# Optimization experiments

Hardware: AMD Instinct MI355X
Metric: run time of the kernel (lower is better)

The kernel has to match this reference:

```python
import jax, jax.numpy as jnp
import numpy as np

B, S, D, H, NL, DF = 32, 512, 512, 8, 6, 2048
E = D // H
EPS = 1e-5

def _pos_emb(s, d):
    pos = np.arange(s, dtype=np.float32)[:, None]
    div = np.exp(np.arange(0, d, 2, dtype=np.float32) * (-np.log(10000.0) / d))
    pe = np.zeros((s, d), np.float32)
    pe[:, 0::2] = np.sin(pos * div)
    pe[:, 1::2] = np.cos(pos * div)
    return jnp.asarray(pe)

PE = _pos_emb(S, D)

def _ln(x, g, b):
    m = jnp.mean(x, -1, keepdims=True)
    v = jnp.var(x, -1, keepdims=True)
    return (x - m) * jax.lax.rsqrt(v + EPS) * g + b

def _cconv(x, w):
    # x: [B, C, L]; w: [O, C, 3]; Conv1d kernel=3, circular padding=1, no bias
    xp = jnp.concatenate([x[..., -1:], x, x[..., :1]], axis=-1)
    return jax.lax.conv_general_dilated(xp, w, (1,), 'VALID', dimension_numbers=('NCH', 'OIH', 'NCH'))

def _projector(x, stats, wc, w1, b1, w2, b2, w3):
    # x: [B, S, C]; stats: [B, 1, C] -> [B, out_dim]
    y = _cconv(x, wc)                                                 # [B, 1, C]
    y = jnp.concatenate([y, stats], axis=1).reshape(x.shape[0], -1)   # [B, 2C]
    y = jax.nn.relu(y @ w1.T + b1)
    y = jax.nn.relu(y @ w2.T + b2)
    return y @ w3.T

def setup_inputs():
    key = jax.random.key(0)
    ks = iter(jax.random.split(key, 48))
    r = lambda *s: jax.random.normal(next(ks), s, jnp.float32) * 0.02
    z = lambda *s: jnp.zeros(s, jnp.float32)
    o = lambda *s: jnp.ones(s, jnp.float32)
    return {
        'x_enc': jax.random.normal(next(ks), (B, S, 2), jnp.float32),
        'W_emb': r(D, 2, 3),
        'Wq': r(NL, D, D), 'bq': z(NL, D),
        'Wk': r(NL, D, D), 'bk': z(NL, D),
        'Wv': r(NL, D, D), 'bv': z(NL, D),
        'Wo': r(NL, D, D), 'bo': z(NL, D),
        'Wc1': r(NL, DF, D), 'bc1': z(NL, DF),
        'Wc2': r(NL, D, DF), 'bc2': z(NL, D),
        'g1': o(NL, D), 'be1': z(NL, D),
        'g2': o(NL, D), 'be2': z(NL, D),
        'gn': o(D), 'bn': z(D),
        'Wout': r(1, D), 'bout': z(1),
        'Wtc': r(1, S, 3), 'Wt1': r(128, 4), 'bt1': z(128), 'Wt2': r(128, 128), 'bt2': z(128), 'Wt3': r(1, 128),
        'Wdc': r(1, S, 3), 'Wd1': r(128, 4), 'bd1': z(128), 'Wd2': r(128, 128), 'bd2': z(128), 'Wd3': r(S, 128),
    }

def reference(x_enc, W_emb, Wq, bq, Wk, bk, Wv, bv, Wo, bo, Wc1, bc1, Wc2, bc2,
              g1, be1, g2, be2, gn, bn, Wout, bout,
              Wtc, Wt1, bt1, Wt2, bt2, Wt3, Wdc, Wd1, bd1, Wd2, bd2, Wd3):
    b = x_enc.shape[0]
    # de-stationary statistics (detached in the original)
    x_raw = jax.lax.stop_gradient(x_enc)
    mean_enc = jax.lax.stop_gradient(jnp.mean(x_enc, 1, keepdims=True))          # [B,1,2]
    std_enc = jax.lax.stop_gradient(jnp.sqrt(jnp.var(x_enc, 1, keepdims=True) + EPS))  # [B,1,2]
    tau = jnp.exp(_projector(x_raw, std_enc, Wtc, Wt1, bt1, Wt2, bt2, Wt3))      # [B,1]
    delta = _projector(x_raw, mean_enc, Wdc, Wd1, bd1, Wd2, bd2, Wd3)            # [B,S]
    tau4 = tau[:, :, None, None]       # [B,1,1,1]
    delta4 = delta[:, None, None, :]   # [B,1,1,S]

    # DataEmbedding: token conv (circular) + sinusoidal positional embedding
    x = _cconv(x_enc.transpose(0, 2, 1), W_emb).transpose(0, 2, 1) + PE[None]    # [B,S,D]

    scale = 1.0 / jnp.sqrt(jnp.float32(E))
    for l in range(NL):
        q = (x @ Wq[l].T + bq[l]).reshape(b, S, H, E)
        k = (x @ Wk[l].T + bk[l]).reshape(b, S, H, E)
        v = (x @ Wv[l].T + bv[l]).reshape(b, S, H, E)
        # DSAttention: rescale scores by tau, shift by delta, then scaled softmax
        scores = jnp.einsum('blhe,bshe->bhls', q, k) * tau4 + delta4
        A = jax.nn.softmax(scale * scores, axis=-1)
        attn = jnp.einsum('bhls,bshe->blhe', A, v).reshape(b, S, D)
        x = _ln(x + attn @ Wo[l].T + bo[l], g1[l], be1[l])
        y = jax.nn.gelu(x @ Wc1[l].T + bc1[l], approximate=False)
        y = y @ Wc2[l].T + bc2[l]
        x = _ln(x + y, g2[l], be2[l])
    x = _ln(x, gn, bn)
    out = jax.nn.gelu(x, approximate=False) @ Wout.T + bout  # [B,S,1]
    return out[..., 0]  # squeeze(-1) -> [B,S]
```

## Files before the change

### kernel.cpp

```cpp
#include <hip/hip_runtime.h>
#include <math.h>

#define Bb 32
#define Ss 512
#define Dd 512
#define Hh 8
#define NLn 6
#define DFf 2048

typedef unsigned short u16;
typedef __attribute__((ext_vector_type(8))) short bf16x8;
typedef __attribute__((ext_vector_type(4))) float f32x4;

__device__ __forceinline__ u16 f2bf(float f){
  union { float f; unsigned u; } x; x.f = f;
  return (u16)((x.u + 0x7fffu + ((x.u >> 16) & 1u)) >> 16);
}
__device__ __forceinline__ float gelu_f(float x){
  return 0.5f * x * (1.0f + erff(x * 0.7071067811865475f));
}
__device__ __forceinline__ f32x4 mfma16(bf16x8 a, bf16x8 b, f32x4 c){
  return __builtin_amdgcn_mfma_f32_16x16x32_bf16(a, b, c, 0, 0, 0);
}
__device__ __forceinline__ void gload16(const void* g, void* l){
  void* gg = (void*)g;
  __builtin_amdgcn_global_load_lds((__attribute__((address_space(1))) void*)gg,
                                   (__attribute__((address_space(3))) void*)l, 16, 0, 0);
}

__global__ void cast_kernel(const float* __restrict__ src, u16* __restrict__ dst, int n){
  int i = (blockIdx.x * 256 + threadIdx.x) * 4;
  if (i < n){
    float4 v = *(const float4*)&src[i];
    ushort4 o; o.x = f2bf(v.x); o.y = f2bf(v.y); o.z = f2bf(v.z); o.w = f2bf(v.w);
    *(ushort4*)&dst[i] = o;
  }
}

__global__ void cast_qkv_kernel(const float* __restrict__ src, u16* __restrict__ dst, int blk){
  int i = (blockIdx.x * 256 + threadIdx.x) * 4;
  if (i < NLn*Dd*Dd){
    int l = i >> 18, r = i & (Dd*Dd - 1);
    float4 v = *(const float4*)&src[i];
    ushort4 o; o.x = f2bf(v.x); o.y = f2bf(v.y); o.z = f2bf(v.z); o.w = f2bf(v.w);
    *(ushort4*)&dst[(size_t)l*(3*Dd*Dd) + (size_t)blk*Dd*Dd + r] = o;
  }
}

__global__ void bias_concat_kernel(const float* __restrict__ bq, const float* __restrict__ bk,
                                   const float* __restrict__ bv, float* __restrict__ dst){
  int i = blockIdx.x*256 + threadIdx.x;
  if (i < NLn*Dd){
    int l = i >> 9, r = i & 511;
    float* d = dst + (size_t)l*1536;
    d[r] = bq[i]; d[512+r] = bk[i]; d[1024+r] = bv[i];
  }
}

#define SCL 0.180336880542795f
__global__ void proj_kernel(const float* __restrict__ x_enc,
                            const float* __restrict__ Wtc, const float* __restrict__ Wt1, const float* __restrict__ bt1,
                            const float* __restrict__ Wt2, const float* __restrict__ bt2, const float* __restrict__ Wt3,
                            const float* __restrict__ Wdc, const float* __restrict__ Wd1, const float* __restrict__ bd1,
                            const float* __restrict__ Wd2, const float* __restrict__ bd2, const float* __restrict__ Wd3,
                            float* __restrict__ tau2, float* __restrict__ delta2){
  const int b = blockIdx.x, t = threadIdx.x;
  __shared__ float red[8][128];
  __shared__ float fv[8];
  __shared__ float ftau[4], fdel[4], h1t[128], h1d[128], h2t[128], h2d[128];
  float s0=0,s1=0,q0=0,q1=0,tc0=0,tc1=0,dc0=0,dc1=0;
  for (int s = t; s < Ss; s += 128){
    float x0 = x_enc[(b*Ss + s)*2 + 0];
    float x1 = x_enc[(b*Ss + s)*2 + 1];
    float wt0 = Wtc[s*3], wt1v = Wtc[s*3+1], wt2v = Wtc[s*3+2];
    float wd0 = Wdc[s*3], wd1v = Wdc[s*3+1], wd2v = Wdc[s*3+2];
    s0 += x0; s1 += x1; q0 += x0*x0; q1 += x1*x1;
    tc0 += x1*(wt0+wt2v) + x0*wt1v;
    tc1 += x0*(wt0+wt2v) + x1*wt1v;
    dc0 += x1*(wd0+wd2v) + x0*wd1v;
    dc1 += x0*(wd0+wd2v) + x1*wd1v;
  }
  red[0][t]=s0; red[1][t]=s1; red[2][t]=q0; red[3][t]=q1;
  red[4][t]=tc0; red[5][t]=tc1; red[6][t]=dc0; red[7][t]=dc1;
  __syncthreads();
  if (t < 8){ float a = 0; for (int i = 0; i < 128; i++) a += red[t][i]; fv[t] = a; }
  __syncthreads();
  if (t == 0){
    float m0 = fv[0]/Ss, m1 = fv[1]/Ss;
    float v0 = fv[2]/Ss - m0*m0, v1 = fv[3]/Ss - m1*m1;
    ftau[0]=fv[4]; ftau[1]=fv[5]; ftau[2]=sqrtf(v0+1e-5f); ftau[3]=sqrtf(v1+1e-5f);
    fdel[0]=fv[6]; fdel[1]=fv[7]; fdel[2]=m0; fdel[3]=m1;
  }
  __syncthreads();
  {
    float a = bt1[t], ad = bd1[t];
    #pragma unroll
    for (int j = 0; j < 4; j++){ a += Wt1[t*4+j]*ftau[j]; ad += Wd1[t*4+j]*fdel[j]; }
    h1t[t] = fmaxf(a, 0.f); h1d[t] = fmaxf(ad, 0.f);
  }
  __syncthreads();
  {
    float a = bt2[t], ad = bd2[t];
    for (int j = 0; j < 128; j++){ a += Wt2[t*128+j]*h1t[j]; ad += Wd2[t*128+j]*h1d[j]; }
    h2t[t] = fmaxf(a, 0.f); h2d[t] = fmaxf(ad, 0.f);
  }
  __syncthreads();
  if (t == 0){
    float z = 0; for (int j = 0; j < 128; j++) z += Wt3[j]*h2t[j];
    tau2[b] = expf(z) * SCL;
  }
  for (int s = t; s < Ss; s += 128){
    float z = 0; for (int j = 0; j < 128; j++) z += Wd3[s*128+j]*h2d[j];
    delta2[b*Ss + s] = z * SCL - 16.0f;
  }
}

__global__ void embed_kernel(const float* __restrict__ xe, const float* __restrict__ Wemb,
                             float* __restrict__ xf, u16* __restrict__ xb){
  const int bs = blockIdx.x;
  const int b = bs >> 9, s = bs & 511;
  const int t = threadIdx.x;
  const int sm = (s + 511) & 511, sp = (s + 1) & 511;
  const float xm0 = xe[(b*Ss + sm)*2],   xm1 = xe[(b*Ss + sm)*2 + 1];
  const float x00 = xe[(b*Ss + s )*2],   x01 = xe[(b*Ss + s )*2 + 1];
  const float xp0 = xe[(b*Ss + sp)*2],   xp1 = xe[(b*Ss + sp)*2 + 1];
  #pragma unroll
  for (int dd = 0; dd < 4; dd++){
    const int d = t*4 + dd;
    const float* wd = Wemb + d*6;
    float a = xm0*wd[0] + x00*wd[1] + xp0*wd[2]
            + xm1*wd[3] + x01*wd[4] + xp1*wd[5];
    const int i2 = d & ~1;
    float div = expf((float)i2 * (-9.210340371976184f / 512.0f));
    float ang = (float)s * div;
    float pe = (d & 1) ? cosf(ang) : sinf(ang);
    float v = a + pe;
    xf[(size_t)bs*Dd + d] = v;
    xb[(size_t)bs*Dd + d] = f2bf(v);
  }
}

template<int EPI>
__global__ __launch_bounds__(256) void gemm_bt(const u16* __restrict__ A, const u16* __restrict__ W,
                                               const float* __restrict__ bias, void* __restrict__ Cv,
                                               int M, int N, int K){
  __shared__ __attribute__((aligned(16))) u16 As[128*32];
  __shared__ __attribute__((aligned(16))) u16 Bs[128*32];
  const int tid = threadIdx.x;
  const int w = tid >> 6, l = tid & 63;
  const int wr = w >> 1, wc = w & 1;
  const long bm0 = (long)blockIdx.y * 128;
  const long bn0 = (long)blockIdx.x * 128;
  const int lr = l >> 2, lc = l & 3;
  const u16* Ag = A + (bm0 + w*32 + lr) * (long)K + lc*8;
  const u16* Bg = W + (bn0 + w*32 + lr) * (long)K + lc*8;
  u16* AsW = As + w*1024;
  u16* BsW = Bs + w*1024;
  f32x4 acc[4][4] = {};
  const int aro = wr*64 + (l & 15);
  const int bro = wc*64 + (l & 15);
  const int k8 = (l >> 4) * 8;
  for (int kt = 0; kt < K; kt += 32){
    gload16(Ag + kt,               AsW);
    gload16(Ag + kt + 16*(long)K,  AsW + 512);
    gload16(Bg + kt,               BsW);
    gload16(Bg + kt + 16*(long)K,  BsW + 512);
    __syncthreads();
    bf16x8 af[4], bfv[4];
    #pragma unroll
    for (int mi = 0; mi < 4; mi++) af[mi] = *(const bf16x8*)&As[(aro + mi*16)*32 + k8];
    #pragma unroll
    for (int ni = 0; ni < 4; ni++) bfv[ni] = *(const bf16x8*)&Bs[(bro + ni*16)*32 + k8];
    #pragma unroll
    for (int mi = 0; mi < 4; mi++)
      #pragma unroll
      for (int ni = 0; ni < 4; ni++)
        acc[mi][ni] = mfma16(af[mi], bfv[ni], acc[mi][ni]);
    __syncthreads();
  }
  const long rbase = bm0 + wr*64 + (l >> 4)*4;
  const int cbase = (int)bn0 + wc*64 + (l & 15);
  #pragma unroll
  for (int ni = 0; ni < 4; ni++){
    const int c = cbase + ni*16;
    const float bvv = bias[c];
    #pragma unroll
    for (int mi = 0; mi < 4; mi++){
      #pragma unroll
      for (int j = 0; j < 4; j++){
        float v = acc[mi][ni][j] + bvv;
        if (EPI == 2) v = gelu_f(v);
        const size_t idx = (size_t)(rbase + mi*16 + j) * N + c;
        if (EPI == 0) ((float*)Cv)[idx] = v;
        else          ((u16*)Cv)[idx]  = f2bf(v);
      }
    }
  }
}

__global__ __launch_bounds__(512, 2) void attn_kernel(const u16* __restrict__ qkv,
                                                      const float* __restrict__ tau2,
                                                      const float* __restrict__ delta2,
                                                      u16* __restrict__ Ob){
  const int bid = blockIdx.x;
  const int h = bid & 7, b = bid >> 3;
  const int t = threadIdx.x, w = t >> 6, l = t & 63;
  const int l15 = l & 15, l4 = l >> 4;
  __shared__ __attribute__((aligned(16))) u16 Ks[512*64];
  __shared__ __attribute__((aligned(16))) u16 Vt[64*520];
  __shared__ __attribute__((aligned(16))) u16 Ps[8][16*72];
  const size_t qkvbase = ((size_t)b*Ss)*1536 + h*64;
  {
    const u16* Kg = qkv + qkvbase + 512  + (size_t)t*1536;
    const u16* Vg = qkv + qkvbase + 1024 + (size_t)t*1536;
    #pragma unroll
    for (int c = 0; c < 8; c++){
      bf16x8 kv = *(const bf16x8*)&Kg[c*8];
      const int byte = t*128 + ((c*16) ^ ((t & 7) << 4));
      *(bf16x8*)((char*)Ks + byte) = kv;
    }
    union { bf16x8 v[8]; u16 e[64]; } vv;
    #pragma unroll
    for (int c = 0; c < 8; c++) vv.v[c] = *(const bf16x8*)&Vg[c*8];
    #pragma unroll
    for (int e = 0; e < 64; e++) Vt[e*520 + t] = vv.e[e];
  }
  const int q0 = w*64;
  bf16x8 qa[4][2];
  #pragma unroll
  for (int mi = 0; mi < 4; mi++)
    #pragma unroll
    for (int ks = 0; ks < 2; ks++)
      qa[mi][ks] = *(const bf16x8*)&qkv[qkvbase + (size_t)(q0 + mi*16 + l15)*1536 + ks*32 + l4*8];
  const float ts = tau2[b];
  bf16x8 ones8;
  #pragma unroll
  for (int i = 0; i < 8; i++) ones8[i] = (short)0x3F80;
  __syncthreads();

  f32x4 Oa[4][4] = {};
  f32x4 Ls[4] = {};
  u16* PsW = Ps[w];
  for (int kt = 0; kt < 8; kt++){
    f32x4 sc[4][4] = {};
    #pragma unroll
    for (int ni = 0; ni < 4; ni++){
      const int krow = kt*64 + ni*16 + l15;
      const int swz = (krow & 7) << 4;
      bf16x8 kf0 = *(const bf16x8*)((const char*)Ks + krow*128 + ((l4*16)      ^ swz));
      bf16x8 kf1 = *(const bf16x8*)((const char*)Ks + krow*128 + ((64 + l4*16) ^ swz));
      #pragma unroll
      for (int mi = 0; mi < 4; mi++){
        sc[mi][ni] = mfma16(qa[mi][0], kf0, sc[mi][ni]);
        sc[mi][ni] = mfma16(qa[mi][1], kf1, sc[mi][ni]);
      }
    }
    float dl[4];
    #pragma unroll
    for (int ni = 0; ni < 4; ni++) dl[ni] = delta2[b*Ss + kt*64 + ni*16 + l15];
    bf16x8 pa[4][2];
    #pragma unroll
    for (int mi = 0; mi < 4; mi++){
      #pragma unroll
      for (int ni = 0; ni < 4; ni++){
        #pragma unroll
        for (int j = 0; j < 4; j++){
          float p = exp2f(ts * sc[mi][ni][j] + dl[ni]);
          PsW[(l4*4 + j)*72 + ni*16 + l15] = f2bf(p);
        }
      }
      pa[mi][0] = *(const bf16x8*)&PsW[l15*72 +      l4*8];
      pa[mi][1] = *(const bf16x8*)&PsW[l15*72 + 32 + l4*8];
    }
    #pragma unroll
    for (int ni = 0; ni < 4; ni++){
      const int vrow = ni*16 + l15;
      bf16x8 vf0 = *(const bf16x8*)&Vt[vrow*520 + kt*64 +      l4*8];
      bf16x8 vf1 = *(const bf16x8*)&Vt[vrow*520 + kt*64 + 32 + l4*8];
      #pragma unroll
      for (int mi = 0; mi < 4; mi++){
        Oa[mi][ni] = mfma16(pa[mi][0], vf0, Oa[mi][ni]);
        Oa[mi][ni] = mfma16(pa[mi][1], vf1, Oa[mi][ni]);
      }
    }
    #pragma unroll
    for (int mi = 0; mi < 4; mi++){
      Ls[mi] = mfma16(pa[mi][0], ones8, Ls[mi]);
      Ls[mi] = mfma16(pa[mi][1], ones8, Ls[mi]);
    }
  }
  const size_t obase = (size_t)b*Ss*Dd + h*64;
  #pragma unroll
  for (int mi = 0; mi < 4; mi++){
    f32x4 rv;
    #pragma unroll
    for (int j = 0; j < 4; j++) rv[j] = 1.0f / Ls[mi][j];
    #pragma unroll
    for (int ni = 0; ni < 4; ni++)
      #pragma unroll
      for (int j = 0; j < 4; j++)
        Ob[obase + (size_t)(q0 + mi*16 + l4*4 + j)*Dd + ni*16 + l15] = f2bf(Oa[mi][ni][j] * rv[j]);
  }
}

__global__ void ln_residual_kernel(float* __restrict__ xf, const float* __restrict__ tf,
                                   const float* __restrict__ g, const float* __restrict__ bln,
                                   u16* __restrict__ xb){
  const int row = blockIdx.x, t = threadIdx.x;
  const size_t base = (size_t)row * Dd + t*4;
  float4 a = *(const float4*)&xf[base];
  const float4 dv = *(const float4*)&tf[base];
  a.x += dv.x; a.y += dv.y; a.z += dv.z; a.w += dv.w;
  float sum = a.x + a.y + a.z + a.w;
  float sq  = a.x*a.x + a.y*a.y + a.z*a.z + a.w*a.w;
  #pragma unroll
  for (int off = 32; off >= 1; off >>= 1){ sum += __shfl_down(sum, off); sq += __shfl_down(sq, off); }
  __shared__ float sh[4];
  const int w = t >> 6, l = t & 63;
  if (l == 0){ sh[w] = sum; sh[2+w] = sq; }
  __syncthreads();
  sum = sh[0] + sh[1]; sq = sh[2] + sh[3];
  const float mean = sum * (1.f/Dd);
  const float var  = sq * (1.f/Dd) - mean*mean;
  const float rstd = rsqrtf(var + 1e-5f);
  const float4 gg = *(const float4*)&g[t*4];
  const float4 bb = *(const float4*)&bln[t*4];
  float4 y;
  y.x = (a.x - mean)*rstd*gg.x + bb.x;
  y.y = (a.y - mean)*rstd*gg.y + bb.y;
  y.z = (a.z - mean)*rstd*gg.z + bb.z;
  y.w = (a.w - mean)*rstd*gg.w + bb.w;
  *(float4*)&xf[base] = y;
  ushort4 o; o.x = f2bf(y.x); o.y = f2bf(y.y); o.z = f2bf(y.z); o.w = f2bf(y.w);
  *(ushort4*)&xb[base] = o;
}

__global__ void final_kernel(const float* __restrict__ xf, const float* __restrict__ gn, const float* __restrict__ bn,
                             const float* __restrict__ Wout, const float* __restrict__ bout,
                             float* __restrict__ out){
  const int row = blockIdx.x, t = threadIdx.x;
  const size_t base = (size_t)row * Dd;
  const int i = t*2;
  float x0 = xf[base+i], x1 = xf[base+i+1];
  float sum = x0 + x1, sq = x0*x0 + x1*x1;
  #pragma unroll
  for (int off = 32; off >= 1; off >>= 1){ sum += __shfl_down(sum, off); sq += __shfl_down(sq, off); }
  __shared__ float sh[8];
  __shared__ float sh2[4];
  const int w = t >> 6, l = t & 63;
  if (l == 0){ sh[w] = sum; sh[4+w] = sq; }
  __syncthreads();
  sum = sh[0]+sh[1]+sh[2]+sh[3];
  sq  = sh[4]+sh[5]+sh[6]+sh[7];
  const float mean = sum * (1.f/Dd);
  const float var  = sq * (1.f/Dd) - mean*mean;
  const float rstd = rsqrtf(var + 1e-5f);
  float y0 = (x0 - mean)*rstd*gn[i]   + bn[i];
  float y1 = (x1 - mean)*rstd*gn[i+1] + bn[i+1];
  float p = gelu_f(y0)*Wout[i] + gelu_f(y1)*Wout[i+1];
  #pragma unroll
  for (int off = 32; off >= 1; off >>= 1) p += __shfl_down(p, off);
  if (l == 0) sh2[w] = p;
  __syncthreads();
  if (t == 0) out[row] = sh2[0]+sh2[1]+sh2[2]+sh2[3] + bout[0];
}

extern "C" void kernel_launch(void* const* d_in, const int* in_sizes, int n_in,
                              void* d_out, int out_size, void* d_ws, size_t ws_size,
                              hipStream_t stream){
  (void)in_sizes; (void)n_in; (void)out_size; (void)ws_size;
  const float* x_enc = (const float*)d_in[0];
  const float* W_emb = (const float*)d_in[1];
  const float* Wq  = (const float*)d_in[2];
  const float* bq  = (const float*)d_in[3];
  const float* Wk  = (const float*)d_in[4];
  const float* bk  = (const float*)d_in[5];
  const float* Wv  = (const float*)d_in[6];
  const float* bvp = (const float*)d_in[7];
  const float* Wo  = (const float*)d_in[8];
  const float* bo  = (const float*)d_in[9];
  const float* Wc1 = (const float*)d_in[10];
  const float* bc1 = (const float*)d_in[11];
  const float* Wc2 = (const float*)d_in[12];
  const float* bc2 = (const float*)d_in[13];
  const float* g1  = (const float*)d_in[14];
  const float* be1 = (const float*)d_in[15];
  const float* g2  = (const float*)d_in[16];
  const float* be2 = (const float*)d_in[17];
  const float* gn  = (const float*)d_in[18];
  const float* bn  = (const float*)d_in[19];
  const float* Wout= (const float*)d_in[20];
  const float* bout= (const float*)d_in[21];
  const float* Wtc = (const float*)d_in[22];
  const float* Wt1 = (const float*)d_in[23];
  const float* bt1 = (const float*)d_in[24];
  const float* Wt2 = (const float*)d_in[25];
  const float* bt2 = (const float*)d_in[26];
  const float* Wt3 = (const float*)d_in[27];
  const float* Wdc = (const float*)d_in[28];
  const float* Wd1 = (const float*)d_in[29];
  const float* bd1 = (const float*)d_in[30];
  const float* Wd2 = (const float*)d_in[31];
  const float* bd2 = (const float*)d_in[32];
  const float* Wd3 = (const float*)d_in[33];

  char* ws = (char*)d_ws;
  size_t off = 0;
  auto alloc = [&](size_t nbytes) -> void* {
    void* p = ws + off; off += (nbytes + 255) & ~(size_t)255; return p;
  };
  const size_t BSD = (size_t)Bb*Ss*Dd;
  u16* Wqkv_b = (u16*)alloc((size_t)NLn*3*Dd*Dd*2);
  u16* Wo_b   = (u16*)alloc((size_t)NLn*Dd*Dd*2);
  u16* Wc1_b  = (u16*)alloc((size_t)NLn*DFf*Dd*2);
  u16* Wc2_b  = (u16*)alloc((size_t)NLn*Dd*DFf*2);
  float* bqkv = (float*)alloc((size_t)NLn*3*Dd*4);
  float* xf   = (float*)alloc(BSD*4);
  u16*   xb   = (u16*)alloc(BSD*2);
  u16*   qkvb = (u16*)alloc(BSD*3*2);
  u16*   ab   = (u16*)alloc(BSD*2);
  float* tf   = (float*)alloc(BSD*4);
  u16*   hb   = (u16*)alloc((size_t)Bb*Ss*DFf*2);
  float* tau2   = (float*)alloc(Bb*4);
  float* delta2 = (float*)alloc((size_t)Bb*Ss*4);

  const int nW = NLn*Dd*Dd;
  const int nC = NLn*DFf*Dd;
  cast_qkv_kernel<<<nW/1024, 256, 0, stream>>>(Wq, Wqkv_b, 0);
  cast_qkv_kernel<<<nW/1024, 256, 0, stream>>>(Wk, Wqkv_b, 1);
  cast_qkv_kernel<<<nW/1024, 256, 0, stream>>>(Wv, Wqkv_b, 2);
  cast_kernel<<<nW/1024, 256, 0, stream>>>(Wo,  Wo_b,  nW);
  cast_kernel<<<nC/1024, 256, 0, stream>>>(Wc1, Wc1_b, nC);
  cast_kernel<<<nC/1024, 256, 0, stream>>>(Wc2, Wc2_b, nC);
  bias_concat_kernel<<<(NLn*Dd + 255)/256, 256, 0, stream>>>(bq, bk, bvp, bqkv);

  proj_kernel<<<Bb, 128, 0, stream>>>(x_enc, Wtc, Wt1, bt1, Wt2, bt2, Wt3,
                                      Wdc, Wd1, bd1, Wd2, bd2, Wd3, tau2, delta2);
  embed_kernel<<<Bb*Ss, 128, 0, stream>>>(x_enc, W_emb, xf, xb);

  const int M = Bb*Ss;
  dim3 gqkv(3*Dd/128, M/128);
  dim3 g512(Dd/128, M/128);
  dim3 g2048(DFf/128, M/128);
  for (int lyr = 0; lyr < NLn; lyr++){
    const u16* wqkv = Wqkv_b + (size_t)lyr*3*Dd*Dd;
    const u16* wo = Wo_b  + (size_t)lyr*Dd*Dd;
    const u16* w1 = Wc1_b + (size_t)lyr*DFf*Dd;
    const u16* w2 = Wc2_b + (size_t)lyr*Dd*DFf;
    gemm_bt<1><<<gqkv, 256, 0, stream>>>(xb, wqkv, bqkv + (size_t)lyr*3*Dd, qkvb, M, 3*Dd, Dd);
    attn_kernel<<<Bb*Hh, 512, 0, stream>>>(qkvb, tau2, delta2, ab);
    gemm_bt<0><<<g512, 256, 0, stream>>>(ab, wo, bo + lyr*Dd, tf, M, Dd, Dd);
    ln_residual_kernel<<<M, 128, 0, stream>>>(xf, tf, g1 + lyr*Dd, be1 + lyr*Dd, xb);
    gemm_bt<2><<<g2048, 256, 0, stream>>>(xb, w1, bc1 + lyr*DFf, hb, M, DFf, Dd);
    gemm_bt<0><<<g512, 256, 0, stream>>>(hb, w2, bc2 + lyr*Dd, tf, M, Dd, DFf);
    ln_residual_kernel<<<M, 128, 0, stream>>>(xf, tf, g2 + lyr*Dd, be2 + lyr*Dd, xb);
  }
  final_kernel<<<M, 256, 0, stream>>>(xf, gn, bn, Wout, bout, (float*)d_out);
}
```

Before: 1.886 ms.

## Double-buffer GEMM LDS tiles, swizzle layout, remap blocks per XCD, stage bf16 stores

The GEMM kernel now double-buffers its shared-memory tiles, so the next K-slice's global-to-LDS loads overlap the current slice's MFMAs, with one barrier per iteration instead of two. The LDS column chunks are XOR-swizzled to cut bank conflicts. A 1D grid is remapped so consecutive tiles land on the same XCD, improving L2 reuse. bf16 epilogues are staged through LDS so each thread writes 16-byte rows instead of scattered 2-byte stores. The cost is doubled LDS use (32KB) and the mapping assumes the block count divides by 8.

```diff
diff --git a/kernel.cpp b/kernel.cpp
--- a/kernel.cpp
+++ b/kernel.cpp
@@ -143,56 +143,116 @@
 template<int EPI>
 __global__ __launch_bounds__(256) void gemm_bt(const u16* __restrict__ A, const u16* __restrict__ W,
                                                const float* __restrict__ bias, void* __restrict__ Cv,
-                                               int M, int N, int K){
-  __shared__ __attribute__((aligned(16))) u16 As[128*32];
-  __shared__ __attribute__((aligned(16))) u16 Bs[128*32];
+                                               int M, int N, int K, int ntx){
+  __shared__ __attribute__((aligned(16))) u16 SM[4*4096];
   const int tid = threadIdx.x;
   const int w = tid >> 6, l = tid & 63;
   const int wr = w >> 1, wc = w & 1;
-  const long bm0 = (long)blockIdx.y * 128;
-  const long bn0 = (long)blockIdx.x * 128;
+  const int nwg = gridDim.x;
+  const int cpx = nwg >> 3;
+  const int lin = blockIdx.x;
+  const int g = (lin & 7)*cpx + (lin >> 3);
+  const int by = g / ntx;
+  const int bx = g - by*ntx;
+  const long bm0 = (long)by * 128;
+  const long bn0 = (long)bx * 128;
   const int lr = l >> 2, lc = l & 3;
-  const u16* Ag = A + (bm0 + w*32 + lr) * (long)K + lc*8;
-  const u16* Bg = W + (bn0 + w*32 + lr) * (long)K + lc*8;
-  u16* AsW = As + w*1024;
-  u16* BsW = Bs + w*1024;
+  const int lcs = lc ^ (lr & 3);
+  const u16* Ag = A + (bm0 + w*32 + lr) * (long)K + lcs*8;
+  const u16* Bg = W + (bn0 + w*32 + lr) * (long)K + lcs*8;
+  u16* AsW[2] = { SM + w*1024,            SM + 2*4096 + w*1024 };
+  u16* BsW[2] = { SM + 4096 + w*1024,     SM + 3*4096 + w*1024 };
   f32x4 acc[4][4] = {};
   const int aro = wr*64 + (l & 15);
   const int bro = wc*64 + (l & 15);
-  const int k8 = (l >> 4) * 8;
-  for (int kt = 0; kt < K; kt += 32){
-    gload16(Ag + kt,               AsW);
-    gload16(Ag + kt + 16*(long)K,  AsW + 512);
-    gload16(Bg + kt,               BsW);
-    gload16(Bg + kt + 16*(long)K,  BsW + 512);
-    __syncthreads();
+  const int ks8 = ((l >> 4) ^ (l & 3)) * 8;
+  gload16(Ag,               AsW[0]);
+  gload16(Ag + 16*(long)K,  AsW[0] + 512);
+  gload16(Bg,               BsW[0]);
+  gload16(Bg + 16*(long)K,  BsW[0] + 512);
+  asm volatile("s_waitcnt vmcnt(0)" ::: "memory");
+  __builtin_amdgcn_s_barrier();
+  asm volatile("" ::: "memory");
+  int cur = 0;
+  for (int kt = 32; kt < K; kt += 32){
+    const int nb = cur ^ 1;
+    gload16(Ag + kt,               AsW[nb]);
+    gload16(Ag + kt + 16*(long)K,  AsW[nb] + 512);
+    gload16(Bg + kt,               BsW[nb]);
+    gload16(Bg + kt + 16*(long)K,  BsW[nb] + 512);
+    const u16* Abuf = SM + cur*2*4096;
+    const u16* Bbuf = Abuf + 4096;
     bf16x8 af[4], bfv[4];
     #pragma unroll
-    for (int mi = 0; mi < 4; mi++) af[mi] = *(const bf16x8*)&As[(aro + mi*16)*32 + k8];
-    #pragma unroll
-    for (int ni = 0; ni < 4; ni++) bfv[ni] = *(const bf16x8*)&Bs[(bro + ni*16)*32 + k8];
+    for (int mi = 0; mi < 4; mi++) af[mi] = *(const bf16x8*)&Abuf[(aro + mi*16)*32 + ks8];
+    #pragma unroll
+    for (int ni = 0; ni < 4; ni++) bfv[ni] = *(const bf16x8*)&Bbuf[(bro + ni*16)*32 + ks8];
     #pragma unroll
     for (int mi = 0; mi < 4; mi++)
       #pragma unroll
       for (int ni = 0; ni < 4; ni++)
         acc[mi][ni] = mfma16(af[mi], bfv[ni], acc[mi][ni]);
-    __syncthreads();
-  }
-  const long rbase = bm0 + wr*64 + (l >> 4)*4;
-  const int cbase = (int)bn0 + wc*64 + (l & 15);
-  #pragma unroll
-  for (int ni = 0; ni < 4; ni++){
-    const int c = cbase + ni*16;
-    const float bvv = bias[c];
-    #pragma unroll
-    for (int mi = 0; mi < 4; mi++){
-      #pragma unroll
-      for (int j = 0; j < 4; j++){
-        float v = acc[mi][ni][j] + bvv;
-        if (EPI == 2) v = gelu_f(v);
-        const size_t idx = (size_t)(rbase + mi*16 + j) * N + c;
-        if (EPI == 0) ((float*)Cv)[idx] = v;
-        else          ((u16*)Cv)[idx]  = f2bf(v);
+    asm volatile("s_waitcnt vmcnt(0)" ::: "memory");
+    __builtin_amdgcn_s_barrier();
+    asm volatile("" ::: "memory");
+    cur = nb;
+  }
+  {
+    const u16* Abuf = SM + cur*2*4096;
+    const u16* Bbuf = Abuf + 4096;
+    bf16x8 af[4], bfv[4];
+    #pragma unroll
+    for (int mi = 0; mi < 4; mi++) af[mi] = *(const bf16x8*)&Abuf[(aro + mi*16)*32 + ks8];
+    #pragma unroll
+    for (int ni = 0; ni < 4; ni++) bfv[ni] = *(const bf16x8*)&Bbuf[(bro + ni*16)*32 + ks8];
+    #pragma unroll
+    for (int mi = 0; mi < 4; mi++)
+      #pragma unroll
+      for (int ni = 0; ni < 4; ni++)
+        acc[mi][ni] = mfma16(af[mi], bfv[ni], acc[mi][ni]);
+  }
+  if (EPI == 0){
+    const long rbase = bm0 + wr*64 + (l >> 4)*4;
+    const int cbase = (int)bn0 + wc*64 + (l & 15);
+    #pragma unroll
+    for (int ni = 0; ni < 4; ni++){
+      const int c = cbase + ni*16;
+      const float bvv = bias[c];
+      #pragma unroll
+      for (int mi = 0; mi < 4; mi++)
+        #pragma unroll
+        for (int j = 0; j < 4; j++)
+          ((float*)Cv)[(size_t)(rbase + mi*16 + j) * N + c] = acc[mi][ni][j] + bvv;
+    }
+  } else {
+    u16* CT = SM;
+    float bvv[4];
+    #pragma unroll
+    for (int ni = 0; ni < 4; ni++) bvv[ni] = bias[bn0 + wc*64 + ni*16 + (l & 15)];
+    u16* Cu = (u16*)Cv;
+    #pragma unroll
+    for (int h = 0; h < 2; h++){
+      __syncthreads();
+      #pragma unroll
+      for (int mi2 = 0; mi2 < 2; mi2++){
+        const int mi = 2*h + mi2;
+        #pragma unroll
+        for (int ni = 0; ni < 4; ni++){
+          #pragma unroll
+          for (int j = 0; j < 4; j++){
+            float v = acc[mi][ni][j] + bvv[ni];
+            if (EPI == 2) v = gelu_f(v);
+            CT[(wr*32 + mi2*16 + (l >> 4)*4 + j)*128 + wc*64 + ni*16 + (l & 15)] = f2bf(v);
+          }
+        }
+      }
+      __syncthreads();
+      #pragma unroll
+      for (int p = 0; p < 4; p++){
+        const int r = (tid >> 4) + p*16;
+        const long grow = bm0 + (r >> 5)*64 + h*32 + (r & 31);
+        *(bf16x8*)&Cu[(size_t)grow * N + bn0 + (tid & 15)*8] =
+            *(const bf16x8*)&CT[r*128 + (tid & 15)*8];
       }
     }
   }
@@ -439,20 +499,20 @@
   embed_kernel<<<Bb*Ss, 128, 0, stream>>>(x_enc, W_emb, xf, xb);
 
   const int M = Bb*Ss;
-  dim3 gqkv(3*Dd/128, M/128);
-  dim3 g512(Dd/128, M/128);
-  dim3 g2048(DFf/128, M/128);
+  const int nQKV = (3*Dd/128)*(M/128);
+  const int n512 = (Dd/128)*(M/128);
+  const int nFF1 = (DFf/128)*(M/128);
   for (int lyr = 0; lyr < NLn; lyr++){
     const u16* wqkv = Wqkv_b + (size_t)lyr*3*Dd*Dd;
     const u16* wo = Wo_b  + (size_t)lyr*Dd*Dd;
     const u16* w1 = Wc1_b + (size_t)lyr*DFf*Dd;
     const u16* w2 = Wc2_b + (size_t)lyr*Dd*DFf;
-    gemm_bt<1><<<gqkv, 256, 0, stream>>>(xb, wqkv, bqkv + (size_t)lyr*3*Dd, qkvb, M, 3*Dd, Dd);
+    gemm_bt<1><<<nQKV, 256, 0, stream>>>(xb, wqkv, bqkv + (size_t)lyr*3*Dd, qkvb, M, 3*Dd, Dd, 3*Dd/128);
     attn_kernel<<<Bb*Hh, 512, 0, stream>>>(qkvb, tau2, delta2, ab);
-    gemm_bt<0><<<g512, 256, 0, stream>>>(ab, wo, bo + lyr*Dd, tf, M, Dd, Dd);
+    gemm_bt<0><<<n512, 256, 0, stream>>>(ab, wo, bo + lyr*Dd, tf, M, Dd, Dd, Dd/128);
     ln_residual_kernel<<<M, 128, 0, stream>>>(xf, tf, g1 + lyr*Dd, be1 + lyr*Dd, xb);
-    gemm_bt<2><<<g2048, 256, 0, stream>>>(xb, w1, bc1 + lyr*DFf, hb, M, DFf, Dd);
-    gemm_bt<0><<<g512, 256, 0, stream>>>(hb, w2, bc2 + lyr*Dd, tf, M, Dd, DFf);
+    gemm_bt<2><<<nFF1, 256, 0, stream>>>(xb, w1, bc1 + lyr*DFf, hb, M, DFf, Dd, DFf/128);
+    gemm_bt<0><<<n512, 256, 0, stream>>>(hb, w2, bc2 + lyr*Dd, tf, M, Dd, DFf, Dd/128);
     ln_residual_kernel<<<M, 128, 0, stream>>>(xf, tf, g2 + lyr*Dd, be2 + lyr*Dd, xb);
   }
   final_kernel<<<M, 256, 0, stream>>>(xf, gn, bn, Wout, bout, (float*)d_out);
```

Result: faster. 1.762 ms (-6.6%).
